# Performance work log

Measured on AMD Instinct MI355X. Metric: run time of the kernel, lower is better.

Reference implementation:

```python
import jax, jax.numpy as jnp
import numpy as np

B, C, D, H, W = 1, 64, 24, 24, 24
N = D * H * W
K = D + H + W - 2  # cross neighbors per node (self deduped)
DS, GD = 64, 64    # d_sim, g_dim
GROUPS = C // 4
EPS = 1e-5
N_ITERS = 2        # pool_strides = [1, 1]


def _build_nbr_idx():
    i, j, k = np.meshgrid(np.arange(D), np.arange(H), np.arange(W), indexing='ij')
    i, j, k = i.reshape(-1), j.reshape(-1), k.reshape(-1)
    a0 = (j * W + k)[:, None] + np.arange(D)[None, :] * (H * W)      # (N, D) full depth line (incl self)
    full1 = (i * H * W + k)[:, None] + np.arange(H)[None, :] * W     # (N, H)
    a1 = full1[np.arange(H)[None, :] != j[:, None]].reshape(N, H - 1)
    full2 = (i * H * W + j * W)[:, None] + np.arange(W)[None, :]     # (N, W)
    a2 = full2[np.arange(W)[None, :] != k[:, None]].reshape(N, W - 1)
    return np.concatenate([a0, a1, a2], axis=1).astype(np.int32)     # (N, K)


def setup_inputs() -> dict:
    key = jax.random.key(0)
    ks = jax.random.split(key, 8)
    s = 0.05
    return {
        'x': jax.random.normal(ks[0], (B, C, D, H, W), jnp.float32),
        'nbr_idx': jnp.asarray(_build_nbr_idx()),
        'phi_w': jax.random.normal(ks[1], (DS, C), jnp.float32) * s,
        'phi_b': jnp.zeros((DS,), jnp.float32),
        'theta_w': jax.random.normal(ks[2], (DS, C), jnp.float32) * s,
        'theta_b': jnp.zeros((DS,), jnp.float32),
        'G_w': jax.random.normal(ks[3], (GD, C), jnp.float32) * s,
        'G_b': jnp.zeros((GD,), jnp.float32),
        'r_w': jax.random.normal(ks[4], (C, GD), jnp.float32) * s,
        'r_b': jnp.zeros((C,), jnp.float32),
        'gn_gamma': jnp.ones((N_ITERS, C), jnp.float32),
        'gn_beta': jnp.zeros((N_ITERS, C), jnp.float32),
        'bn_gamma': jnp.ones((C,), jnp.float32),
        'bn_beta': jnp.zeros((C,), jnp.float32),
        'bn_mean': jnp.zeros((C,), jnp.float32),
        'bn_var': jnp.ones((C,), jnp.float32),
    }


def _group_norm(v, gamma, beta):
    vg = v.reshape(B, GROUPS, C // GROUPS, D, H, W)
    m = vg.mean(axis=(2, 3, 4, 5), keepdims=True)
    var = ((vg - m) ** 2).mean(axis=(2, 3, 4, 5), keepdims=True)
    vn = ((vg - m) / jnp.sqrt(var + EPS)).reshape(B, C, D, H, W)
    return vn * gamma[None, :, None, None, None] + beta[None, :, None, None, None]


def reference(x, nbr_idx, phi_w, phi_b, theta_w, theta_b, G_w, G_b, r_w, r_b,
              gn_gamma, gn_beta, bn_gamma, bn_beta, bn_mean, bn_var):
    h = x
    for it in range(N_ITERS):
        hf = h.reshape(B, C, N).transpose(2, 0, 1)                    # (N, B, C) node features
        theta = jnp.einsum('nbc,dc->nbd', hf, theta_w) + theta_b     # (N, B, DS) queries
        phi_all = jnp.einsum('nbc,dc->nbd', hf, phi_w) + phi_b       # (N, B, DS) keys (pre-gather)
        g_all = jnp.einsum('nbc,gc->nbg', hf, G_w) + G_b             # (N, B, GD) values (pre-gather)
        phi_e = phi_all[nbr_idx]                                      # (N, K, B, DS) mailbox gather
        g_e = g_all[nbr_idx]                                          # (N, K, B, GD)
        f = jnp.einsum('nbd,nkbd->nbk', theta, phi_e)                # attention logits over K
        a = jax.nn.softmax(f, axis=-1)                                # non_local_merge 'softmax'
        y = jnp.einsum('nbk,nkbg->nbg', a, g_e)                      # weighted value sum
        cross = jnp.einsum('nbg,cg->nbc', y, r_w) + r_b              # (N, B, C) output proj
        cross = cross.transpose(1, 2, 0).reshape(B, C, D, H, W)
        h = h + _group_norm(cross, gn_gamma[it], gn_beta[it])
    # BatchNorm3d (eval, running stats) + ReLU
    bc = lambda v: v[None, :, None, None, None]
    out = (h - bc(bn_mean)) / jnp.sqrt(bc(bn_var) + EPS) * bc(bn_gamma) + bc(bn_beta)
    return jax.nn.relu(out)
```

## Files before the change

### kernel.cpp

```cpp
#include <hip/hip_runtime.h>
#include <math.h>

#define NN 13824
#define LW 24

__global__ __launch_bounds__(256) void apply_proj_kernel(
    const float* __restrict__ x,
    const float* __restrict__ cross, const float* __restrict__ gsum,
    const float* __restrict__ gn_g, const float* __restrict__ gn_b,
    float* __restrict__ h_out, int mode,
    const float* __restrict__ phi_w, const float* __restrict__ phi_b,
    const float* __restrict__ theta_w, const float* __restrict__ theta_b,
    const float* __restrict__ g_w, const float* __restrict__ g_b,
    float* __restrict__ theta, float* __restrict__ phi, float* __restrict__ gv)
{
    __shared__ float hs[64 * 64];
    __shared__ float wos[64 * 196];

    const int tid = threadIdx.x;
    const int n0 = blockIdx.x * 64;

    if (mode == 1) {
        for (int i = tid; i < 4096; i += 256) {
            int nl = i >> 6, c = i & 63;
            wos[c * 65 + nl] = cross[(size_t)(n0 + nl) * 64 + c];
        }
        __syncthreads();
        const float inv_cnt = 1.f / 55296.f;
        for (int i = tid; i < 4096; i += 256) {
            int c = i >> 6, nl = i & 63;
            int gr = c >> 2;
            float mean = gsum[gr * 16] * inv_cnt;
            float var = gsum[512 + gr * 16] * inv_cnt - mean * mean;
            float v = (wos[c * 65 + nl] - mean) * rsqrtf(var + 1e-5f) * gn_g[c] + gn_b[c];
            size_t o = (size_t)c * NN + n0 + nl;
            float hv = x[o] + v;
            hs[c * 64 + nl] = hv;
            h_out[o] = hv;
        }
        __syncthreads();
    } else {
        for (int i = tid; i < 4096; i += 256) {
            int c = i >> 6, nl = i & 63;
            hs[c * 64 + nl] = x[(size_t)c * NN + n0 + nl];
        }
    }

    for (int i = tid; i < 64 * 192; i += 256) {
        int d = i >> 6;
        int c = i & 63;
        const float* src; int dd;
        if (d < 64)       { src = theta_w; dd = d; }
        else if (d < 128) { src = phi_w;   dd = d - 64; }
        else              { src = g_w;     dd = d - 128; }
        wos[c * 196 + d] = src[dd * 64 + c];
    }
    __syncthreads();

    const int nl0 = (tid & 15) * 4;
    const int d0  = (tid >> 4) * 12;

    float acc[4][12];
    #pragma unroll
    for (int q = 0; q < 4; q++)
        #pragma unroll
        for (int j = 0; j < 12; j++) acc[q][j] = 0.f;

    #pragma unroll 2
    for (int c = 0; c < 64; c++) {
        float4 hv = *(const float4*)&hs[c * 64 + nl0];
        float w[12];
        *(float4*)&w[0] = *(const float4*)&wos[c * 196 + d0];
        *(float4*)&w[4] = *(const float4*)&wos[c * 196 + d0 + 4];
        *(float4*)&w[8] = *(const float4*)&wos[c * 196 + d0 + 8];
        #pragma unroll
        for (int j = 0; j < 12; j++) {
            acc[0][j] += hv.x * w[j];
            acc[1][j] += hv.y * w[j];
            acc[2][j] += hv.z * w[j];
            acc[3][j] += hv.w * w[j];
        }
    }
    __syncthreads();
    #pragma unroll
    for (int q = 0; q < 4; q++)
        #pragma unroll
        for (int j = 0; j < 12; j++)
            wos[(nl0 + q) * 196 + d0 + j] = acc[q][j];
    __syncthreads();

    for (int i = tid; i < 3 * 64 * 64; i += 256) {
        int dd = i & 63;
        int rest = i >> 6;
        int nl = rest & 63;
        int t = rest >> 6;
        float v = wos[nl * 196 + t * 64 + dd];
        size_t o = (size_t)(n0 + nl) * 64 + dd;
        if (t == 0)      theta[o] = v + theta_b[dd];
        else if (t == 1) phi[o]   = v + phi_b[dd];
        else             gv[o]    = v + g_b[dd];
    }
}

__global__ __launch_bounds__(256) void line_attn_kernel(
    const float* __restrict__ theta,
    const float* __restrict__ phi,
    const float* __restrict__ gv,
    float* __restrict__ y_part,
    float* __restrict__ l_part,
    float* __restrict__ gsum)
{
    __shared__ float th[LW * 68], ph[LW * 68], gs[LW * 68];
    __shared__ float P[LW * 28];
    __shared__ float lrow[LW];

    const int tid = threadIdx.x;
    const int axis = blockIdx.x / 576;
    const int L = blockIdx.x % 576;

    if (blockIdx.x == 0) {
        for (int i = tid; i < 1024; i += 256) gsum[i] = 0.f;
    }

    int base, stride;
    if (axis == 0)      { base = L * 24;                    stride = 1;   }
    else if (axis == 1) { base = (L / 24) * 576 + (L % 24); stride = 24;  }
    else                { base = L;                         stride = 576; }
    const bool excl = (axis != 2);

    for (int e = tid; e < LW * 64; e += 256) {
        int r = e >> 6, d = e & 63;
        size_t g = (size_t)(base + r * stride) * 64 + d;
        th[r * 68 + d] = theta[g];
        ph[r * 68 + d] = phi[g];
        gs[r * 68 + d] = gv[g];
    }
    __syncthreads();

    for (int e = tid; e < 576; e += 256) {
        int r = e % 24, c = e / 24;
        float s = 0.f;
        #pragma unroll 8
        for (int d = 0; d < 64; d++) s += th[r * 68 + d] * ph[c * 68 + d];
        P[r * 28 + c] = (excl && r == c) ? 0.f : __expf(s);
    }
    __syncthreads();

    if (tid < 192) {
        int r = tid >> 3, q = tid & 7;
        float s = P[r * 28 + q] + P[r * 28 + q + 8] + P[r * 28 + q + 16];
        s += __shfl_xor(s, 1);
        s += __shfl_xor(s, 2);
        s += __shfl_xor(s, 4);
        if (q == 0) lrow[r] = s;
    }
    __syncthreads();

    float* yp = y_part + (size_t)axis * NN * 64;
    float* lp = l_part + (size_t)axis * NN;
    const int d = tid & 63, w = tid >> 6;
    float acc[6];
    #pragma unroll
    for (int q = 0; q < 6; q++) acc[q] = 0.f;
    #pragma unroll 4
    for (int c = 0; c < 24; c++) {
        float gval = gs[c * 68 + d];
        #pragma unroll
        for (int q = 0; q < 6; q++) acc[q] += P[(w + 4 * q) * 28 + c] * gval;
    }
    #pragma unroll
    for (int q = 0; q < 6; q++) {
        int r = w + 4 * q;
        size_t n = (size_t)(base + r * stride);
        yp[n * 64 + d] = acc[q];
    }
    if (tid < 24) lp[(size_t)(base + tid * stride)] = lrow[tid];
}

__global__ __launch_bounds__(256) void combine_kernel(
    const float* __restrict__ y_part, const float* __restrict__ l_part,
    const float* __restrict__ r_w, const float* __restrict__ r_b,
    float* __restrict__ cross, float* __restrict__ gsum)
{
    __shared__ float ys[16 * 68];
    __shared__ float red_s[4][64], red_ss[4][64];

    const int tid = threadIdx.x;
    const int d = tid & 63, w = tid >> 6;
    const int n0 = blockIdx.x * 16;
    const size_t S = (size_t)NN * 64;

    #pragma unroll
    for (int q = 0; q < 4; q++) {
        int nn = w * 4 + q;
        int n = n0 + nn;
        float lv = l_part[n] + l_part[NN + n] + l_part[2 * NN + n];
        size_t o = (size_t)n * 64 + d;
        float yv = y_part[o] + y_part[S + o] + y_part[2 * S + o];
        ys[nn * 68 + d] = yv / lv;
    }
    __syncthreads();

    const int c = d;
    float rb = r_b[c];
    float acc[4] = {rb, rb, rb, rb};
    for (int dd = 0; dd < 64; dd += 4) {
        float4 r4 = *(const float4*)&r_w[c * 64 + dd];
        #pragma unroll
        for (int q = 0; q < 4; q++) {
            float4 y4 = *(const float4*)&ys[(w * 4 + q) * 68 + dd];
            acc[q] += r4.x * y4.x + r4.y * y4.y + r4.z * y4.z + r4.w * y4.w;
        }
    }
    float s = 0.f, ss = 0.f;
    #pragma unroll
    for (int q = 0; q < 4; q++) {
        int n = n0 + w * 4 + q;
        cross[(size_t)n * 64 + c] = acc[q];
        s += acc[q];
        ss += acc[q] * acc[q];
    }
    red_s[w][c] = s;
    red_ss[w][c] = ss;
    __syncthreads();
    if (w == 0) {
        float ts  = red_s[0][c] + red_s[1][c] + red_s[2][c] + red_s[3][c];
        float tss = red_ss[0][c] + red_ss[1][c] + red_ss[2][c] + red_ss[3][c];
        ts  += __shfl_xor(ts, 1);  ts  += __shfl_xor(ts, 2);
        tss += __shfl_xor(tss, 1); tss += __shfl_xor(tss, 2);
        if ((c & 3) == 0) {
            atomicAdd(&gsum[(c >> 2) * 16], ts);
            atomicAdd(&gsum[512 + (c >> 2) * 16], tss);
        }
    }
}

__global__ __launch_bounds__(256) void final_kernel(
    const float* __restrict__ cross,
    const float* __restrict__ gsum,
    const float* __restrict__ gn_g, const float* __restrict__ gn_b,
    const float* __restrict__ h_in,
    const float* __restrict__ bn_g, const float* __restrict__ bn_b,
    const float* __restrict__ bn_m, const float* __restrict__ bn_v,
    float* __restrict__ out)
{
    __shared__ float t[64 * 65];
    const int tid = threadIdx.x;
    const int n0 = blockIdx.x * 64;
    for (int i = tid; i < 4096; i += 256) {
        int nl = i >> 6, c = i & 63;
        t[c * 65 + nl] = cross[(size_t)(n0 + nl) * 64 + c];
    }
    __syncthreads();
    const float inv_cnt = 1.f / 55296.f;
    for (int i = tid; i < 4096; i += 256) {
        int c = i >> 6, nl = i & 63;
        int gr = c >> 2;
        float mean = gsum[gr * 16] * inv_cnt;
        float var = gsum[512 + gr * 16] * inv_cnt - mean * mean;
        float v = (t[c * 65 + nl] - mean) * rsqrtf(var + 1e-5f) * gn_g[c] + gn_b[c];
        size_t o = (size_t)c * NN + n0 + nl;
        float h2 = h_in[o] + v;
        float bnv = (h2 - bn_m[c]) * rsqrtf(bn_v[c] + 1e-5f) * bn_g[c] + bn_b[c];
        out[o] = fmaxf(bnv, 0.f);
    }
}

extern "C" void kernel_launch(void* const* d_in, const int* in_sizes, int n_in,
                              void* d_out, int out_size, void* d_ws, size_t ws_size,
                              hipStream_t stream)
{
    const float* x        = (const float*)d_in[0];
    const float* phi_w    = (const float*)d_in[2];
    const float* phi_b    = (const float*)d_in[3];
    const float* theta_w  = (const float*)d_in[4];
    const float* theta_b  = (const float*)d_in[5];
    const float* G_w      = (const float*)d_in[6];
    const float* G_b      = (const float*)d_in[7];
    const float* r_w      = (const float*)d_in[8];
    const float* r_b      = (const float*)d_in[9];
    const float* gn_gamma = (const float*)d_in[10];
    const float* gn_beta  = (const float*)d_in[11];
    const float* bn_gamma = (const float*)d_in[12];
    const float* bn_beta  = (const float*)d_in[13];
    const float* bn_mean  = (const float*)d_in[14];
    const float* bn_var   = (const float*)d_in[15];

    float* ws = (float*)d_ws;
    const size_t S = (size_t)NN * 64;
    float* h1    = ws;
    float* tc    = ws + S;
    float* phi   = ws + 2 * S;
    float* gv    = ws + 3 * S;
    float* ypart = ws + 4 * S;
    float* lpart = ws + 7 * S;
    float* gsum  = ws + 7 * S + 3 * NN;

    apply_proj_kernel<<<216, 256, 0, stream>>>(x, tc, gsum, gn_gamma, gn_beta,
                                               h1, 0,
                                               phi_w, phi_b, theta_w, theta_b,
                                               G_w, G_b, tc, phi, gv);
    line_attn_kernel<<<1728, 256, 0, stream>>>(tc, phi, gv, ypart, lpart, gsum);
    combine_kernel<<<864, 256, 0, stream>>>(ypart, lpart, r_w, r_b, tc, gsum);
    apply_proj_kernel<<<216, 256, 0, stream>>>(x, tc, gsum, gn_gamma, gn_beta,
                                               h1, 1,
                                               phi_w, phi_b, theta_w, theta_b,
                                               G_w, G_b, tc, phi, gv);
    line_attn_kernel<<<1728, 256, 0, stream>>>(tc, phi, gv, ypart, lpart, gsum);
    combine_kernel<<<864, 256, 0, stream>>>(ypart, lpart, r_w, r_b, tc, gsum);
    final_kernel<<<216, 256, 0, stream>>>(tc, gsum, gn_gamma + 64, gn_beta + 64,
                                          h1, bn_gamma, bn_beta, bn_mean, bn_var,
                                          (float*)d_out);
}
```

Baseline: 237.0 us.

## Split projection by output matrix and make line attention one wavefront per line

The projection kernel now launches three blocks per 64-node tile, one each for theta, phi and g. This triples the block count, shrinks shared memory, and writes outputs directly with float4 stores instead of staging through shared memory. The line-attention kernel gives each 64-lane wavefront its own line, with two lines per 128-thread block. It loads with float4, computes 3x3 register tiles of the logits, and drops the __syncthreads barriers by relying on intra-wavefront ordering. Cross is moved to a separate buffer so theta no longer aliases it, and mode-1 blocks recompute the GroupNorm residual three times.

```diff
diff --git a/kernel.cpp b/kernel.cpp
--- a/kernel.cpp
+++ b/kernel.cpp
@@ -9,21 +9,31 @@
     const float* __restrict__ cross, const float* __restrict__ gsum,
     const float* __restrict__ gn_g, const float* __restrict__ gn_b,
     float* __restrict__ h_out, int mode,
+    const float* __restrict__ theta_w, const float* __restrict__ theta_b,
     const float* __restrict__ phi_w, const float* __restrict__ phi_b,
-    const float* __restrict__ theta_w, const float* __restrict__ theta_b,
     const float* __restrict__ g_w, const float* __restrict__ g_b,
     float* __restrict__ theta, float* __restrict__ phi, float* __restrict__ gv)
 {
     __shared__ float hs[64 * 64];
-    __shared__ float wos[64 * 196];
+    __shared__ float ws[64 * 68];
 
     const int tid = threadIdx.x;
-    const int n0 = blockIdx.x * 64;
-
-    if (mode == 1) {
+    const int tile = blockIdx.x / 3, ts = blockIdx.x % 3;
+    const int n0 = tile * 64;
+
+    const float* wsel = (ts == 0) ? theta_w : (ts == 1) ? phi_w : g_w;
+    const float* bsel = (ts == 0) ? theta_b : (ts == 1) ? phi_b : g_b;
+    float*       osel = (ts == 0) ? theta   : (ts == 1) ? phi   : gv;
+
+    if (mode == 0) {
+        for (int i = tid; i < 4096; i += 256) {
+            int c = i >> 6, nl = i & 63;
+            hs[c * 64 + nl] = x[(size_t)c * NN + n0 + nl];
+        }
+    } else {
         for (int i = tid; i < 4096; i += 256) {
             int nl = i >> 6, c = i & 63;
-            wos[c * 65 + nl] = cross[(size_t)(n0 + nl) * 64 + c];
+            ws[c * 68 + nl] = cross[(size_t)(n0 + nl) * 64 + c];
         }
         __syncthreads();
         const float inv_cnt = 1.f / 55296.f;
@@ -32,77 +42,53 @@
             int gr = c >> 2;
             float mean = gsum[gr * 16] * inv_cnt;
             float var = gsum[512 + gr * 16] * inv_cnt - mean * mean;
-            float v = (wos[c * 65 + nl] - mean) * rsqrtf(var + 1e-5f) * gn_g[c] + gn_b[c];
+            float v = (ws[c * 68 + nl] - mean) * rsqrtf(var + 1e-5f) * gn_g[c] + gn_b[c];
             size_t o = (size_t)c * NN + n0 + nl;
             float hv = x[o] + v;
             hs[c * 64 + nl] = hv;
-            h_out[o] = hv;
+            if (ts == 0) h_out[o] = hv;
         }
         __syncthreads();
-    } else {
-        for (int i = tid; i < 4096; i += 256) {
-            int c = i >> 6, nl = i & 63;
-            hs[c * 64 + nl] = x[(size_t)c * NN + n0 + nl];
-        }
-    }
-
-    for (int i = tid; i < 64 * 192; i += 256) {
-        int d = i >> 6;
-        int c = i & 63;
-        const float* src; int dd;
-        if (d < 64)       { src = theta_w; dd = d; }
-        else if (d < 128) { src = phi_w;   dd = d - 64; }
-        else              { src = g_w;     dd = d - 128; }
-        wos[c * 196 + d] = src[dd * 64 + c];
+    }
+
+    for (int i = tid; i < 4096; i += 256) {
+        int d = i >> 6, c = i & 63;
+        ws[c * 68 + d] = wsel[d * 64 + c];
     }
     __syncthreads();
 
-    const int nl0 = (tid & 15) * 4;
-    const int d0  = (tid >> 4) * 12;
-
-    float acc[4][12];
+    const int d0  = (tid & 15) * 4;
+    const int nl0 = (tid >> 4) * 4;
+    float acc[4][4];
     #pragma unroll
     for (int q = 0; q < 4; q++)
         #pragma unroll
-        for (int j = 0; j < 12; j++) acc[q][j] = 0.f;
-
-    #pragma unroll 2
+        for (int j = 0; j < 4; j++) acc[q][j] = 0.f;
+
+    #pragma unroll 4
     for (int c = 0; c < 64; c++) {
         float4 hv = *(const float4*)&hs[c * 64 + nl0];
-        float w[12];
-        *(float4*)&w[0] = *(const float4*)&wos[c * 196 + d0];
-        *(float4*)&w[4] = *(const float4*)&wos[c * 196 + d0 + 4];
-        *(float4*)&w[8] = *(const float4*)&wos[c * 196 + d0 + 8];
-        #pragma unroll
-        for (int j = 0; j < 12; j++) {
-            acc[0][j] += hv.x * w[j];
-            acc[1][j] += hv.y * w[j];
-            acc[2][j] += hv.z * w[j];
-            acc[3][j] += hv.w * w[j];
-        }
-    }
-    __syncthreads();
-    #pragma unroll
-    for (int q = 0; q < 4; q++)
-        #pragma unroll
-        for (int j = 0; j < 12; j++)
-            wos[(nl0 + q) * 196 + d0 + j] = acc[q][j];
-    __syncthreads();
-
-    for (int i = tid; i < 3 * 64 * 64; i += 256) {
-        int dd = i & 63;
-        int rest = i >> 6;
-        int nl = rest & 63;
-        int t = rest >> 6;
-        float v = wos[nl * 196 + t * 64 + dd];
-        size_t o = (size_t)(n0 + nl) * 64 + dd;
-        if (t == 0)      theta[o] = v + theta_b[dd];
-        else if (t == 1) phi[o]   = v + phi_b[dd];
-        else             gv[o]    = v + g_b[dd];
-    }
-}
-
-__global__ __launch_bounds__(256) void line_attn_kernel(
+        float4 wv = *(const float4*)&ws[c * 68 + d0];
+        #pragma unroll
+        for (int j = 0; j < 4; j++) {
+            float w = (&wv.x)[j];
+            acc[0][j] += hv.x * w;
+            acc[1][j] += hv.y * w;
+            acc[2][j] += hv.z * w;
+            acc[3][j] += hv.w * w;
+        }
+    }
+    float4 bias = *(const float4*)&bsel[d0];
+    #pragma unroll
+    for (int q = 0; q < 4; q++) {
+        float4 v;
+        v.x = acc[q][0] + bias.x; v.y = acc[q][1] + bias.y;
+        v.z = acc[q][2] + bias.z; v.w = acc[q][3] + bias.w;
+        *(float4*)&osel[(size_t)(n0 + nl0 + q) * 64 + d0] = v;
+    }
+}
+
+__global__ __launch_bounds__(128) void line_attn_kernel(
     const float* __restrict__ theta,
     const float* __restrict__ phi,
     const float* __restrict__ gv,
@@ -110,16 +96,16 @@
     float* __restrict__ l_part,
     float* __restrict__ gsum)
 {
-    __shared__ float th[LW * 68], ph[LW * 68], gs[LW * 68];
-    __shared__ float P[LW * 28];
-    __shared__ float lrow[LW];
+    __shared__ float th[2][LW * 68], ph[2][LW * 68], gs[2][LW * 68];
+    __shared__ float P[2][LW * 28];
 
     const int tid = threadIdx.x;
-    const int axis = blockIdx.x / 576;
-    const int L = blockIdx.x % 576;
+    const int wv = tid >> 6, lane = tid & 63;
+    const int gl = blockIdx.x * 2 + wv;
+    const int axis = gl / 576, L = gl % 576;
 
     if (blockIdx.x == 0) {
-        for (int i = tid; i < 1024; i += 256) gsum[i] = 0.f;
+        for (int i = tid; i < 1024; i += 128) gsum[i] = 0.f;
     }
 
     int base, stride;
@@ -128,53 +114,75 @@
     else                { base = L;                         stride = 576; }
     const bool excl = (axis != 2);
 
-    for (int e = tid; e < LW * 64; e += 256) {
-        int r = e >> 6, d = e & 63;
-        size_t g = (size_t)(base + r * stride) * 64 + d;
-        th[r * 68 + d] = theta[g];
-        ph[r * 68 + d] = phi[g];
-        gs[r * 68 + d] = gv[g];
-    }
-    __syncthreads();
-
-    for (int e = tid; e < 576; e += 256) {
-        int r = e % 24, c = e / 24;
+    #pragma unroll
+    for (int q = 0; q < 6; q++) {
+        int idx = q * 64 + lane;
+        int row = idx >> 4, c4 = (idx & 15) * 4;
+        size_t g = (size_t)(base + row * stride) * 64 + c4;
+        int la = row * 68 + c4;
+        *(float4*)&th[wv][la] = *(const float4*)&theta[g];
+        *(float4*)&ph[wv][la] = *(const float4*)&phi[g];
+        *(float4*)&gs[wv][la] = *(const float4*)&gv[g];
+    }
+
+    const int r0 = (lane >> 3) * 3, c0 = (lane & 7) * 3;
+    float sa[3][3];
+    #pragma unroll
+    for (int a = 0; a < 3; a++)
+        #pragma unroll
+        for (int b = 0; b < 3; b++) sa[a][b] = 0.f;
+
+    #pragma unroll 4
+    for (int d4 = 0; d4 < 64; d4 += 4) {
+        float4 t[3], p[3];
+        #pragma unroll
+        for (int a = 0; a < 3; a++) t[a] = *(const float4*)&th[wv][(r0 + a) * 68 + d4];
+        #pragma unroll
+        for (int b = 0; b < 3; b++) p[b] = *(const float4*)&ph[wv][(c0 + b) * 68 + d4];
+        #pragma unroll
+        for (int a = 0; a < 3; a++)
+            #pragma unroll
+            for (int b = 0; b < 3; b++)
+                sa[a][b] += t[a].x * p[b].x + t[a].y * p[b].y +
+                            t[a].z * p[b].z + t[a].w * p[b].w;
+    }
+    #pragma unroll
+    for (int a = 0; a < 3; a++)
+        #pragma unroll
+        for (int b = 0; b < 3; b++) {
+            float e = (excl && (r0 + a) == (c0 + b)) ? 0.f : __expf(sa[a][b]);
+            P[wv][(r0 + a) * 28 + c0 + b] = e;
+        }
+
+    if (lane < 24) {
         float s = 0.f;
-        #pragma unroll 8
-        for (int d = 0; d < 64; d++) s += th[r * 68 + d] * ph[c * 68 + d];
-        P[r * 28 + c] = (excl && r == c) ? 0.f : __expf(s);
-    }
-    __syncthreads();
-
-    if (tid < 192) {
-        int r = tid >> 3, q = tid & 7;
-        float s = P[r * 28 + q] + P[r * 28 + q + 8] + P[r * 28 + q + 16];
-        s += __shfl_xor(s, 1);
-        s += __shfl_xor(s, 2);
-        s += __shfl_xor(s, 4);
-        if (q == 0) lrow[r] = s;
-    }
-    __syncthreads();
-
+        #pragma unroll
+        for (int c4 = 0; c4 < 24; c4 += 4) {
+            float4 pv = *(const float4*)&P[wv][lane * 28 + c4];
+            s += pv.x + pv.y + pv.z + pv.w;
+        }
+        l_part[(size_t)axis * NN + base + lane * stride] = s;
+    }
+
+    float acc[24];
+    #pragma unroll
+    for (int r = 0; r < 24; r++) acc[r] = 0.f;
+    #pragma unroll
+    for (int c4 = 0; c4 < 24; c4 += 4) {
+        float g0 = gs[wv][(c4 + 0) * 68 + lane];
+        float g1 = gs[wv][(c4 + 1) * 68 + lane];
+        float g2 = gs[wv][(c4 + 2) * 68 + lane];
+        float g3 = gs[wv][(c4 + 3) * 68 + lane];
+        #pragma unroll
+        for (int r = 0; r < 24; r++) {
+            float4 pv = *(const float4*)&P[wv][r * 28 + c4];
+            acc[r] += pv.x * g0 + pv.y * g1 + pv.z * g2 + pv.w * g3;
+        }
+    }
     float* yp = y_part + (size_t)axis * NN * 64;
-    float* lp = l_part + (size_t)axis * NN;
-    const int d = tid & 63, w = tid >> 6;
-    float acc[6];
-    #pragma unroll
-    for (int q = 0; q < 6; q++) acc[q] = 0.f;
-    #pragma unroll 4
-    for (int c = 0; c < 24; c++) {
-        float gval = gs[c * 68 + d];
-        #pragma unroll
-        for (int q = 0; q < 6; q++) acc[q] += P[(w + 4 * q) * 28 + c] * gval;
-    }
-    #pragma unroll
-    for (int q = 0; q < 6; q++) {
-        int r = w + 4 * q;
-        size_t n = (size_t)(base + r * stride);
-        yp[n * 64 + d] = acc[q];
-    }
-    if (tid < 24) lp[(size_t)(base + tid * stride)] = lrow[tid];
+    #pragma unroll
+    for (int r = 0; r < 24; r++)
+        yp[(size_t)(base + r * stride) * 64 + lane] = acc[r];
 }
 
 __global__ __launch_bounds__(256) void combine_kernel(
@@ -289,26 +297,27 @@
     float* ws = (float*)d_ws;
     const size_t S = (size_t)NN * 64;
     float* h1    = ws;
-    float* tc    = ws + S;
+    float* theta = ws + S;
     float* phi   = ws + 2 * S;
     float* gv    = ws + 3 * S;
     float* ypart = ws + 4 * S;
-    float* lpart = ws + 7 * S;
-    float* gsum  = ws + 7 * S + 3 * NN;
-
-    apply_proj_kernel<<<216, 256, 0, stream>>>(x, tc, gsum, gn_gamma, gn_beta,
+    float* cross = ws + 7 * S;
+    float* lpart = ws + 8 * S;
+    float* gsum  = ws + 8 * S + 3 * NN;
+
+    apply_proj_kernel<<<648, 256, 0, stream>>>(x, cross, gsum, gn_gamma, gn_beta,
                                                h1, 0,
-                                               phi_w, phi_b, theta_w, theta_b,
-                                               G_w, G_b, tc, phi, gv);
-    line_attn_kernel<<<1728, 256, 0, stream>>>(tc, phi, gv, ypart, lpart, gsum);
-    combine_kernel<<<864, 256, 0, stream>>>(ypart, lpart, r_w, r_b, tc, gsum);
-    apply_proj_kernel<<<216, 256, 0, stream>>>(x, tc, gsum, gn_gamma, gn_beta,
+                                               theta_w, theta_b, phi_w, phi_b,
+                                               G_w, G_b, theta, phi, gv);
+    line_attn_kernel<<<864, 128, 0, stream>>>(theta, phi, gv, ypart, lpart, gsum);
+    combine_kernel<<<864, 256, 0, stream>>>(ypart, lpart, r_w, r_b, cross, gsum);
+    apply_proj_kernel<<<648, 256, 0, stream>>>(x, cross, gsum, gn_gamma, gn_beta,
                                                h1, 1,
-                                               phi_w, phi_b, theta_w, theta_b,
-                                               G_w, G_b, tc, phi, gv);
-    line_attn_kernel<<<1728, 256, 0, stream>>>(tc, phi, gv, ypart, lpart, gsum);
-    combine_kernel<<<864, 256, 0, stream>>>(ypart, lpart, r_w, r_b, tc, gsum);
-    final_kernel<<<216, 256, 0, stream>>>(tc, gsum, gn_gamma + 64, gn_beta + 64,
+                                               theta_w, theta_b, phi_w, phi_b,
+                                               G_w, G_b, theta, phi, gv);
+    line_attn_kernel<<<864, 128, 0, stream>>>(theta, phi, gv, ypart, lpart, gsum);
+    combine_kernel<<<864, 256, 0, stream>>>(ypart, lpart, r_w, r_b, cross, gsum);
+    final_kernel<<<216, 256, 0, stream>>>(cross, gsum, gn_gamma + 64, gn_beta + 64,
                                           h1, bn_gamma, bn_beta, bn_mean, bn_var,
                                           (float*)d_out);
 }
```

Result: faster. 223.9 us (-5.5%).
